# Optimization experiments

Hardware: AMD Instinct MI355X
Metric: run time of the kernel (lower is better)

## Reference

```python
import jax, jax.numpy as jnp
import numpy as np

B, N, C, H = 2, 4096, 384, 6
HD = C // H          # 64
HALF = C // 2        # 192 = 3 pose heads * HD
MLP_H = 4 * C        # 1536
EPS = 1e-5


def _ln(x, g, b):
    m = jnp.mean(x, axis=-1, keepdims=True)
    v = jnp.mean((x - m) ** 2, axis=-1, keepdims=True)
    return (x - m) * jax.lax.rsqrt(v + EPS) * g + b


def setup_inputs() -> dict:
    key = jax.random.key(0)
    ks = jax.random.split(key, 6)
    s = 0.02
    return {
        "x": jax.random.normal(ks[0], (B, N, C), dtype=jnp.float32),
        "qkv_w": jax.random.normal(ks[1], (3 * C, C), dtype=jnp.float32) * s,
        "proj_w": jax.random.normal(ks[2], (C, HALF), dtype=jnp.float32) * s,
        "proj_b": jnp.zeros((C,), jnp.float32),
        "gamma1": jnp.ones((C,), jnp.float32),
        "beta1": jnp.zeros((C,), jnp.float32),
        "gamma2": jnp.ones((C,), jnp.float32),
        "beta2": jnp.zeros((C,), jnp.float32),
        "fc1_w": jax.random.normal(ks[3], (MLP_H, C), dtype=jnp.float32) * s,
        "fc1_b": jnp.zeros((MLP_H,), jnp.float32),
        "fc2_w": jax.random.normal(ks[4], (C, MLP_H), dtype=jnp.float32) * s,
        "fc2_b": jnp.zeros((C,), jnp.float32),
    }


def reference(x, qkv_w, proj_w, proj_b, gamma1, beta1, gamma2, beta2,
              fc1_w, fc1_b, fc2_w, fc2_b):
    b, n, c = x.shape
    scale = HD ** -0.5
    # --- attention on pre-norm input ---
    h = _ln(x, gamma1, beta1)
    qkv = (h @ qkv_w.T).reshape(b, n, 3, H, HD).transpose(2, 0, 3, 1, 4)  # [3,B,H,N,HD]
    q, k, v = qkv[0], qkv[1], qkv[2]
    # obj heads 0:3 -> sigmoid attention; pose heads 3:6 -> softmax attention
    attn_obj = jax.nn.sigmoid(jnp.einsum('bhnd,bhmd->bhnm', q[:, :3], k[:, :3]) * scale)
    attn_pose = jax.nn.softmax(jnp.einsum('bhnd,bhmd->bhnm', q[:, 3:], k[:, 3:]) * scale, axis=-1)
    # chained combine: pose-attn applied after obj-attn on pose values
    ctx = jnp.einsum('bhnm,bhmd->bhnd', attn_obj, v[:, 3:])      # [B,3,N,HD]
    ctx = jnp.einsum('bhnm,bhmd->bhnd', attn_pose, ctx)          # [B,3,N,HD]
    ctx = ctx.transpose(0, 2, 1, 3).reshape(b, n, HALF)          # [B,N,C/2]
    x = x + (ctx @ proj_w.T + proj_b)
    # --- MLP ---
    h2 = _ln(x, gamma2, beta2)
    mlp = jax.nn.gelu(h2 @ fc1_w.T + fc1_b, approximate=False) @ fc2_w.T + fc2_b
    return (x + mlp, attn_obj)
```

## Files before the change

### kernel.cpp

```cpp
#include <hip/hip_runtime.h>
#include <hip/hip_bf16.h>
#include <cmath>


typedef __hip_bfloat16 bf16;
typedef __attribute__((ext_vector_type(8))) short short8;
typedef __attribute__((ext_vector_type(4))) short s16x4;
typedef __attribute__((ext_vector_type(4))) float f32x4;

#define MFMA16(a, b, c) __builtin_amdgcn_mfma_f32_16x16x32_bf16((a), (b), (c), 0, 0, 0)

__device__ __forceinline__ void async16(const void* g, void* l) {
  __builtin_amdgcn_global_load_lds(
      (const __attribute__((address_space(1))) void*)g,
      (__attribute__((address_space(3))) void*)l, 16, 0, 0);
}

__device__ __forceinline__ short f2bs(float v) {
  union { bf16 b; short s; } u;
  u.b = __float2bfloat16(v);
  return u.s;
}

template <bool FIRST>
__global__ __launch_bounds__(256) void ln_fwd(const float* __restrict__ x,
                                              const float* __restrict__ gamma,
                                              const float* __restrict__ beta,
                                              bf16* __restrict__ out,
                                              const float* __restrict__ w0,
                                              const float* __restrict__ w1,
                                              const float* __restrict__ w2,
                                              const float* __restrict__ w3,
                                              bf16* __restrict__ o0, bf16* __restrict__ o1,
                                              bf16* __restrict__ o2, bf16* __restrict__ o3) {
  const int bx = blockIdx.x;
  if (FIRST) {
    if (bx >= 2048) {
      int i = (bx - 2048) * 256 + threadIdx.x;
      const int n0 = 442368 / 4, n1 = 73728 / 4, n2 = 589824 / 4, n3 = 589824 / 4;
      const float* src;
      bf16* dst;
      if (i < n0) { src = w0; dst = o0; }
      else if ((i -= n0) < n1) { src = w1; dst = o1; }
      else if ((i -= n1) < n2) { src = w2; dst = o2; }
      else { i -= n2; src = w3; dst = o3; }
      f32x4 v = *(const f32x4*)(src + (size_t)i * 4);
      s16x4 o;
#pragma unroll
      for (int e = 0; e < 4; ++e) o[e] = f2bs(v[e]);
      *(s16x4*)(dst + (size_t)i * 4) = o;
      return;
    }
  }
  const int row = bx * 4 + (threadIdx.x >> 6);
  const int l = threadIdx.x & 63;
  const float* xr = x + (size_t)row * 384;
  float v[6];
  float s = 0.f, q = 0.f;
#pragma unroll
  for (int i = 0; i < 6; ++i) {
    v[i] = xr[l + i * 64];
    s += v[i];
    q += v[i] * v[i];
  }
#pragma unroll
  for (int m = 1; m < 64; m <<= 1) {
    s += __shfl_xor(s, m);
    q += __shfl_xor(q, m);
  }
  float mean = s * (1.0f / 384.0f);
  float var = q * (1.0f / 384.0f) - mean * mean;
  float rstd = rsqrtf(var + 1e-5f);
  bf16* orow = out + (size_t)row * 384;
#pragma unroll
  for (int i = 0; i < 6; ++i)
    orow[l + i * 64] = __float2bfloat16((v[i] - mean) * rstd * gamma[l + i * 64] + beta[l + i * 64]);
}

template <int EPI>
__global__ __launch_bounds__(256) void gemm128(const bf16* __restrict__ A,
                                               const bf16* __restrict__ Bm, int M, int N, int K,
                                               const float* __restrict__ bias,
                                               bf16* __restrict__ outb) {
  __shared__ __attribute__((aligned(16))) short As[128][64];
  __shared__ __attribute__((aligned(16))) short Bs[128][64];
  const int t = threadIdx.x;
  const int l = t & 63;
  const int w = t >> 6;
  const int wm = w >> 1, wn = w & 1;
  const int bm = blockIdx.y * 128, bn = blockIdx.x * 128;

  f32x4 acc[4][4] = {};
  const int r8 = t >> 3;
  const int c8 = (t & 7) * 8;
  const bf16* Ab = A + (size_t)(bm + r8) * K + c8;
  const bf16* Bb = Bm + (size_t)(bn + r8) * K + c8;

  for (int kt = 0; kt < K; kt += 64) {
    __syncthreads();
#pragma unroll
    for (int i = 0; i < 4; ++i)
      async16(Ab + (size_t)(i * 32) * K + kt, &As[i * 32 + r8][c8]);
#pragma unroll
    for (int i = 0; i < 4; ++i)
      async16(Bb + (size_t)(i * 32) * K + kt, &Bs[i * 32 + r8][c8]);
    __syncthreads();
#pragma unroll
    for (int ks = 0; ks < 2; ++ks) {
      short8 a[4], b[4];
#pragma unroll
      for (int i = 0; i < 4; ++i)
        a[i] = *(const short8*)&As[wm * 64 + i * 16 + (l & 15)][ks * 32 + (l >> 4) * 8];
#pragma unroll
      for (int i = 0; i < 4; ++i)
        b[i] = *(const short8*)&Bs[wn * 64 + i * 16 + (l & 15)][ks * 32 + (l >> 4) * 8];
#pragma unroll
      for (int i = 0; i < 4; ++i)
#pragma unroll
        for (int j = 0; j < 4; ++j) acc[i][j] = MFMA16(a[i], b[j], acc[i][j]);
    }
  }

#pragma unroll
  for (int i = 0; i < 4; ++i) {
#pragma unroll
    for (int j = 0; j < 4; ++j) {
#pragma unroll
      for (int r = 0; r < 4; ++r) {
        int row = bm + wm * 64 + i * 16 + (l >> 4) * 4 + r;
        int col = bn + wn * 64 + j * 16 + (l & 15);
        float v = acc[i][j][r];
        if (EPI == 0) {
          int three = col / 384;
          int rem = col - three * 384;
          int head = rem >> 6;
          int hd = rem & 63;
          int bb = row >> 12;
          int n = row & 4095;
          const size_t QSZ = (size_t)2 * 6 * 4096 * 64;
          if (three < 2) {
            size_t di = ((((size_t)three * 2 + bb) * 6 + head) * 4096 + n) * 64 + hd;
            outb[di] = __float2bfloat16(v);
          } else {
            size_t di = 2 * QSZ + (((size_t)bb * 6 + head) * 64 + hd) * 4096 + n;
            outb[di] = __float2bfloat16(v);
          }
        } else {
          float u = v + bias[col];
          float z = 0.7978845608f * (u + 0.044715f * u * u * u);
          float e = __builtin_amdgcn_exp2f(z * 2.885390082f);
          float th = 1.0f - 2.0f * __builtin_amdgcn_rcpf(e + 1.0f);
          outb[(size_t)row * N + col] = __float2bfloat16(0.5f * u * (1.0f + th));
        }
      }
    }
  }
}

__global__ __launch_bounds__(256) void gemm64sq(const bf16* __restrict__ A,
                                                const bf16* __restrict__ Bm, int M, int N, int K,
                                                const float* __restrict__ bias,
                                                const float* __restrict__ resid,
                                                float* __restrict__ outf) {
  __shared__ __attribute__((aligned(16))) short As[2][64][64];
  __shared__ __attribute__((aligned(16))) short Bs[2][64][64];
  const int t = threadIdx.x;
  const int l = t & 63;
  const int w = t >> 6;
  const int wm = w >> 1, wn = w & 1;
  const int bm = blockIdx.y * 64, bn = blockIdx.x * 64;
  const int r8 = t >> 3, c8 = (t & 7) * 8;

  const bf16* Ab = A + (size_t)(bm + r8) * K + c8;
  const bf16* Bb = Bm + (size_t)(bn + r8) * K + c8;

  f32x4 acc[2][2] = {};

  auto stage = [&](int kt, int bf) {
    async16(Ab + kt, &As[bf][r8][c8]);
    async16(Ab + (size_t)32 * K + kt, &As[bf][32 + r8][c8]);
    async16(Bb + kt, &Bs[bf][r8][c8]);
    async16(Bb + (size_t)32 * K + kt, &Bs[bf][32 + r8][c8]);
  };

  stage(0, 0);
  int bf = 0;
  for (int kt = 0; kt < K; kt += 64) {
    __syncthreads();
    if (kt + 64 < K) stage(kt + 64, bf ^ 1);
#pragma unroll
    for (int ks = 0; ks < 2; ++ks) {
      short8 a[2], b[2];
#pragma unroll
      for (int i = 0; i < 2; ++i)
        a[i] = *(const short8*)&As[bf][wm * 32 + i * 16 + (l & 15)][ks * 32 + (l >> 4) * 8];
#pragma unroll
      for (int j = 0; j < 2; ++j)
        b[j] = *(const short8*)&Bs[bf][wn * 32 + j * 16 + (l & 15)][ks * 32 + (l >> 4) * 8];
#pragma unroll
      for (int i = 0; i < 2; ++i)
#pragma unroll
        for (int j = 0; j < 2; ++j) acc[i][j] = MFMA16(a[i], b[j], acc[i][j]);
    }
    bf ^= 1;
  }

#pragma unroll
  for (int i = 0; i < 2; ++i) {
#pragma unroll
    for (int j = 0; j < 2; ++j) {
#pragma unroll
      for (int r = 0; r < 4; ++r) {
        int row = bm + wm * 32 + i * 16 + (l >> 4) * 4 + r;
        int col = bn + wn * 32 + j * 16 + (l & 15);
        size_t di = (size_t)row * N + col;
        outf[di] = acc[i][j][r] + bias[col] + resid[di];
      }
    }
  }
}

template <int MODE>
__global__ __launch_bounds__(256) void attn_fused(const bf16* __restrict__ qkvb,
                                                  const bf16* __restrict__ vsrc_base,
                                                  float* __restrict__ aout,
                                                  bf16* __restrict__ outd) {
  const int bh = blockIdx.y, b = bh / 3, h = bh - b * 3;
  const int row0 = blockIdx.x * 64;
  const int t = threadIdx.x, l = t & 63, w = t >> 6;

  const size_t HSZ = (size_t)4096 * 64;
  const size_t QSZ = (size_t)2 * 6 * 4096 * 64;
  const int head = (MODE == 0) ? h : h + 3;
  const bf16* qp = qkvb + (size_t)(b * 6 + head) * HSZ;
  const bf16* kp = qkvb + QSZ + (size_t)(b * 6 + head) * HSZ;
  const bf16* vbase = (MODE == 0)
      ? qkvb + 2 * QSZ + (size_t)((b * 6 + h + 3) * 64) * 4096
      : vsrc_base + (size_t)(bh * 64) * 4096;

  __shared__ __attribute__((aligned(16))) short Ks[2][64][64];
  __shared__ __attribute__((aligned(16))) short Vs[2][64][64];
  __shared__ __attribute__((aligned(16))) float Sf[4][16][68];
  __shared__ float Ls[4][16];

  short8 aq[2];
  {
    int qrow = row0 + w * 16 + (l & 15);
    const bf16* qq = qp + (size_t)qrow * 64 + (l >> 4) * 8;
    aq[0] = *(const short8*)(qq);
    aq[1] = *(const short8*)(qq + 32);
  }

  const int r8 = t >> 3, c8 = (t & 7) * 8;
  const int sc = c8 ^ ((r8 & 7) * 8);

  auto stage = [&](int ct, int bf) {
    const bf16* kb = kp + (size_t)(ct * 64) * 64;
    async16(kb + (size_t)r8 * 64 + sc, &Ks[bf][r8][c8]);
    async16(kb + (size_t)(32 + r8) * 64 + sc, &Ks[bf][32 + r8][c8]);
    const bf16* vb = vbase + ct * 64;
    async16(vb + (size_t)r8 * 4096 + sc, &Vs[bf][r8][c8]);
    async16(vb + (size_t)(32 + r8) * 4096 + sc, &Vs[bf][32 + r8][c8]);
  };

  f32x4 cacc[4] = {};
  float lp[4] = {0.f, 0.f, 0.f, 0.f};
  const float K1 = -0.18033688f;
  const float K2 = 0.18033688f;

  float* sfw = &Sf[w][0][0];
  stage(0, 0);
  int bf = 0;
  for (int ct = 0; ct < 64; ++ct) {
    __syncthreads();
    if (ct < 63) stage(ct + 1, bf ^ 1);

    f32x4 sacc[4] = {};
#pragma unroll
    for (int ks = 0; ks < 2; ++ks) {
      short8 bk[4];
#pragma unroll
      for (int j = 0; j < 4; ++j) {
        int rr = j * 16 + (l & 15);
        int ec = (ks * 32 + (l >> 4) * 8) ^ ((rr & 7) * 8);
        bk[j] = *(const short8*)&Ks[bf][rr][ec];
      }
      __builtin_amdgcn_s_setprio(1);
#pragma unroll
      for (int j = 0; j < 4; ++j) sacc[j] = MFMA16(aq[ks], bk[j], sacc[j]);
      __builtin_amdgcn_s_setprio(0);
    }

#pragma unroll
    for (int j = 0; j < 4; ++j) {
#pragma unroll
      for (int r = 0; r < 4; ++r) {
        float s = sacc[j][r];
        float v;
        if (MODE == 0) {
          v = __builtin_amdgcn_rcpf(1.0f + __builtin_amdgcn_exp2f(s * K1));
        } else {
          v = __builtin_amdgcn_exp2f(s * K2);
          lp[r] += v;
        }
        sfw[((l >> 4) * 4 + r) * 68 + j * 16 + (l & 15)] = v;
      }
    }

    short8 pa[2];
#pragma unroll
    for (int ks = 0; ks < 2; ++ks) {
      const float* sp = &sfw[(l & 15) * 68 + ks * 32 + (l >> 4) * 8];
      f32x4 f0 = *(const f32x4*)sp;
      f32x4 f1 = *(const f32x4*)(sp + 4);
      short8 a;
#pragma unroll
      for (int e = 0; e < 4; ++e) a[e] = f2bs(f0[e]);
#pragma unroll
      for (int e = 0; e < 4; ++e) a[4 + e] = f2bs(f1[e]);
      pa[ks] = a;
    }

    if (MODE == 0) {
      float* ab = aout + (size_t)bh * 4096 * 4096 +
                  (size_t)(row0 + w * 16) * 4096 + ct * 64;
#pragma unroll
      for (int i = 0; i < 4; ++i) {
        f32x4 vv = *(const f32x4*)&sfw[(4 * i + (l >> 4)) * 68 + (l & 15) * 4];
        *(f32x4*)(ab + (size_t)(4 * i + (l >> 4)) * 4096 + (l & 15) * 4) = vv;
      }
    }

#pragma unroll
    for (int ks = 0; ks < 2; ++ks) {
      short8 bv[4];
#pragma unroll
      for (int j = 0; j < 4; ++j) {
        int rr = j * 16 + (l & 15);
        int ec = (ks * 32 + (l >> 4) * 8) ^ ((rr & 7) * 8);
        bv[j] = *(const short8*)&Vs[bf][rr][ec];
      }
      __builtin_amdgcn_s_setprio(1);
#pragma unroll
      for (int j = 0; j < 4; ++j) cacc[j] = MFMA16(pa[ks], bv[j], cacc[j]);
      __builtin_amdgcn_s_setprio(0);
    }
    bf ^= 1;
  }

  if (MODE == 0) {
    __syncthreads();
    short(*S)[66] = (short(*)[66]) & Ks[0][0][0];
#pragma unroll
    for (int j = 0; j < 4; ++j)
#pragma unroll
      for (int r = 0; r < 4; ++r)
        S[w * 16 + (l >> 4) * 4 + r][j * 16 + (l & 15)] = f2bs(cacc[j][r]);
    __syncthreads();
    const int hd = t >> 2, nb = (t & 3) * 16;
    short8 o0, o1;
#pragma unroll
    for (int k = 0; k < 8; ++k) o0[k] = S[nb + k][hd];
#pragma unroll
    for (int k = 0; k < 8; ++k) o1[k] = S[nb + 8 + k][hd];
    short* dst = (short*)(outd + ((size_t)bh * 64 + hd) * 4096 + row0 + nb);
    *(short8*)dst = o0;
    *(short8*)(dst + 8) = o1;
  } else {
#pragma unroll
    for (int r = 0; r < 4; ++r) {
#pragma unroll
      for (int m = 1; m < 16; m <<= 1) lp[r] += __shfl_xor(lp[r], m);
    }
    if ((l & 15) == 0) {
#pragma unroll
      for (int r = 0; r < 4; ++r) Ls[w][(l >> 4) * 4 + r] = lp[r];
    }
#pragma unroll
    for (int j = 0; j < 4; ++j)
#pragma unroll
      for (int r = 0; r < 4; ++r)
        sfw[((l >> 4) * 4 + r) * 68 + j * 16 + (l & 15)] = cacc[j][r];
    const int row = l >> 2, hd0 = (l & 3) * 16;
    float inv = 1.0f / Ls[w][row];
    short8 o[2];
#pragma unroll
    for (int g = 0; g < 4; ++g) {
      f32x4 v = *(const f32x4*)&sfw[row * 68 + hd0 + g * 4];
#pragma unroll
      for (int e = 0; e < 4; ++e) o[g >> 1][(g & 1) * 4 + e] = f2bs(v[e] * inv);
    }
    short* dst = (short*)(outd + ((size_t)b * 4096 + row0 + w * 16 + row) * 192 + h * 64 + hd0);
    *(short8*)dst = o[0];
    *(short8*)(dst + 8) = o[1];
  }
}

extern "C" void kernel_launch(void* const* d_in, const int* in_sizes, int n_in,
                              void* d_out, int out_size, void* d_ws, size_t ws_size,
                              hipStream_t stream) {
  const float* x      = (const float*)d_in[0];
  const float* qkv_w  = (const float*)d_in[1];
  const float* proj_w = (const float*)d_in[2];
  const float* proj_b = (const float*)d_in[3];
  const float* gamma1 = (const float*)d_in[4];
  const float* beta1  = (const float*)d_in[5];
  const float* gamma2 = (const float*)d_in[6];
  const float* beta2  = (const float*)d_in[7];
  const float* fc1_w  = (const float*)d_in[8];
  const float* fc1_b  = (const float*)d_in[9];
  const float* fc2_w  = (const float*)d_in[10];
  const float* fc2_b  = (const float*)d_in[11];

  float* out_x = (float*)d_out;
  float* out_attn = out_x + (size_t)2 * 4096 * 384;

  char* ws = (char*)d_ws;
  size_t off = 0;
  auto alloc = [&](size_t bytes) -> void* {
    void* p = ws + off;
    off += (bytes + 255) & ~(size_t)255;
    return p;
  };
  bf16* qkv_w_b  = (bf16*)alloc((size_t)1152 * 384 * 2);
  bf16* proj_w_b = (bf16*)alloc((size_t)384 * 192 * 2);
  bf16* fc1_w_b  = (bf16*)alloc((size_t)1536 * 384 * 2);
  bf16* fc2_w_b  = (bf16*)alloc((size_t)384 * 1536 * 2);
  bf16* h1    = (bf16*)alloc((size_t)8192 * 384 * 2);
  bf16* qkvb  = (bf16*)alloc((size_t)3 * 2 * 6 * 4096 * 64 * 2);
  bf16* ctx1T = (bf16*)alloc((size_t)6 * 64 * 4096 * 2);
  bf16* ctxf  = (bf16*)alloc((size_t)2 * 4096 * 192 * 2);
  float* x2   = (float*)alloc((size_t)8192 * 384 * 4);
  bf16* h2    = (bf16*)alloc((size_t)8192 * 384 * 2);
  bf16* h3    = (bf16*)alloc((size_t)8192 * 1536 * 2);

  ln_fwd<true><<<3704, 256, 0, stream>>>(x, gamma1, beta1, h1,
                                         qkv_w, proj_w, fc1_w, fc2_w,
                                         qkv_w_b, proj_w_b, fc1_w_b, fc2_w_b);

  gemm128<0><<<dim3(9, 64), 256, 0, stream>>>(h1, qkv_w_b, 8192, 1152, 384,
                                              nullptr, qkvb);

  attn_fused<0><<<dim3(64, 6), 256, 0, stream>>>(qkvb, nullptr, out_attn, ctx1T);
  attn_fused<1><<<dim3(64, 6), 256, 0, stream>>>(qkvb, ctx1T, nullptr, ctxf);

  gemm64sq<<<dim3(6, 128), 256, 0, stream>>>(ctxf, proj_w_b, 8192, 384, 192,
                                             proj_b, x, x2);
  ln_fwd<false><<<2048, 256, 0, stream>>>(x2, gamma2, beta2, h2,
                                          nullptr, nullptr, nullptr, nullptr,
                                          nullptr, nullptr, nullptr, nullptr);
  gemm128<2><<<dim3(12, 64), 256, 0, stream>>>(h2, fc1_w_b, 8192, 1536, 384,
                                               fc1_b, h3);
  gemm64sq<<<dim3(6, 128), 256, 0, stream>>>(h3, fc2_w_b, 8192, 384, 1536,
                                             fc2_b, x2, out_x);
}
```

Measured before the change: 309.0 us.

## Split pose softmax attention over key chunks with partial-sum reduction kernel

The softmax pose attention kernel is split out and parallelised across four key chunks, so the grid grows from 384 to 1536 blocks, which should fill the GPU better. Each block writes unnormalised partial context and row sums, and a new reduce kernel combines them and normalises. The pose kernel also drops LDS staging of K and V and reads fragments straight from global memory. This adds extra fp32 partial-buffer traffic and a kernel launch. Skipping the max subtraction was already the approach before, so numerics are unchanged.

Measured after the change: 417.0 us. 1.35x slower.

```diff
diff --git a/kernel.cpp b/kernel.cpp
--- a/kernel.cpp
+++ b/kernel.cpp
@@ -220,28 +220,22 @@
   }
 }
 
-template <int MODE>
-__global__ __launch_bounds__(256) void attn_fused(const bf16* __restrict__ qkvb,
-                                                  const bf16* __restrict__ vsrc_base,
-                                                  float* __restrict__ aout,
-                                                  bf16* __restrict__ outd) {
+__global__ __launch_bounds__(256) void attn_obj(const bf16* __restrict__ qkvb,
+                                                float* __restrict__ aout,
+                                                bf16* __restrict__ ctx1T) {
   const int bh = blockIdx.y, b = bh / 3, h = bh - b * 3;
   const int row0 = blockIdx.x * 64;
   const int t = threadIdx.x, l = t & 63, w = t >> 6;
 
   const size_t HSZ = (size_t)4096 * 64;
   const size_t QSZ = (size_t)2 * 6 * 4096 * 64;
-  const int head = (MODE == 0) ? h : h + 3;
-  const bf16* qp = qkvb + (size_t)(b * 6 + head) * HSZ;
-  const bf16* kp = qkvb + QSZ + (size_t)(b * 6 + head) * HSZ;
-  const bf16* vbase = (MODE == 0)
-      ? qkvb + 2 * QSZ + (size_t)((b * 6 + h + 3) * 64) * 4096
-      : vsrc_base + (size_t)(bh * 64) * 4096;
+  const bf16* qp = qkvb + (size_t)(b * 6 + h) * HSZ;
+  const bf16* kp = qkvb + QSZ + (size_t)(b * 6 + h) * HSZ;
+  const bf16* vbase = qkvb + 2 * QSZ + (size_t)((b * 6 + h + 3) * 64) * 4096;
 
   __shared__ __attribute__((aligned(16))) short Ks[2][64][64];
   __shared__ __attribute__((aligned(16))) short Vs[2][64][64];
   __shared__ __attribute__((aligned(16))) float Sf[4][16][68];
-  __shared__ float Ls[4][16];
 
   short8 aq[2];
   {
@@ -264,9 +258,7 @@
   };
 
   f32x4 cacc[4] = {};
-  float lp[4] = {0.f, 0.f, 0.f, 0.f};
   const float K1 = -0.18033688f;
-  const float K2 = 0.18033688f;
 
   float* sfw = &Sf[w][0][0];
   stage(0, 0);
@@ -295,14 +287,7 @@
     for (int j = 0; j < 4; ++j) {
 #pragma unroll
       for (int r = 0; r < 4; ++r) {
-        float s = sacc[j][r];
-        float v;
-        if (MODE == 0) {
-          v = __builtin_amdgcn_rcpf(1.0f + __builtin_amdgcn_exp2f(s * K1));
-        } else {
-          v = __builtin_amdgcn_exp2f(s * K2);
-          lp[r] += v;
-        }
+        float v = __builtin_amdgcn_rcpf(1.0f + __builtin_amdgcn_exp2f(sacc[j][r] * K1));
         sfw[((l >> 4) * 4 + r) * 68 + j * 16 + (l & 15)] = v;
       }
     }
@@ -321,7 +306,7 @@
       pa[ks] = a;
     }
 
-    if (MODE == 0) {
+    {
       float* ab = aout + (size_t)bh * 4096 * 4096 +
                   (size_t)(row0 + w * 16) * 4096 + ct * 64;
 #pragma unroll
@@ -348,52 +333,154 @@
     bf ^= 1;
   }
 
-  if (MODE == 0) {
-    __syncthreads();
-    short(*S)[66] = (short(*)[66]) & Ks[0][0][0];
-#pragma unroll
-    for (int j = 0; j < 4; ++j)
-#pragma unroll
-      for (int r = 0; r < 4; ++r)
-        S[w * 16 + (l >> 4) * 4 + r][j * 16 + (l & 15)] = f2bs(cacc[j][r]);
-    __syncthreads();
-    const int hd = t >> 2, nb = (t & 3) * 16;
-    short8 o0, o1;
-#pragma unroll
-    for (int k = 0; k < 8; ++k) o0[k] = S[nb + k][hd];
-#pragma unroll
-    for (int k = 0; k < 8; ++k) o1[k] = S[nb + 8 + k][hd];
-    short* dst = (short*)(outd + ((size_t)bh * 64 + hd) * 4096 + row0 + nb);
-    *(short8*)dst = o0;
-    *(short8*)(dst + 8) = o1;
-  } else {
-#pragma unroll
-    for (int r = 0; r < 4; ++r) {
-#pragma unroll
-      for (int m = 1; m < 16; m <<= 1) lp[r] += __shfl_xor(lp[r], m);
-    }
-    if ((l & 15) == 0) {
-#pragma unroll
-      for (int r = 0; r < 4; ++r) Ls[w][(l >> 4) * 4 + r] = lp[r];
-    }
-#pragma unroll
-    for (int j = 0; j < 4; ++j)
-#pragma unroll
-      for (int r = 0; r < 4; ++r)
-        sfw[((l >> 4) * 4 + r) * 68 + j * 16 + (l & 15)] = cacc[j][r];
-    const int row = l >> 2, hd0 = (l & 3) * 16;
-    float inv = 1.0f / Ls[w][row];
-    short8 o[2];
-#pragma unroll
-    for (int g = 0; g < 4; ++g) {
-      f32x4 v = *(const f32x4*)&sfw[row * 68 + hd0 + g * 4];
-#pragma unroll
-      for (int e = 0; e < 4; ++e) o[g >> 1][(g & 1) * 4 + e] = f2bs(v[e] * inv);
-    }
-    short* dst = (short*)(outd + ((size_t)b * 4096 + row0 + w * 16 + row) * 192 + h * 64 + hd0);
-    *(short8*)dst = o[0];
-    *(short8*)(dst + 8) = o[1];
-  }
+  __syncthreads();
+  short(*S)[66] = (short(*)[66]) & Ks[0][0][0];
+#pragma unroll
+  for (int j = 0; j < 4; ++j)
+#pragma unroll
+    for (int r = 0; r < 4; ++r)
+      S[w * 16 + (l >> 4) * 4 + r][j * 16 + (l & 15)] = f2bs(cacc[j][r]);
+  __syncthreads();
+  const int hd = t >> 2, nb = (t & 3) * 16;
+  short8 o0, o1;
+#pragma unroll
+  for (int k = 0; k < 8; ++k) o0[k] = S[nb + k][hd];
+#pragma unroll
+  for (int k = 0; k < 8; ++k) o1[k] = S[nb + 8 + k][hd];
+  short* dst = (short*)(ctx1T + ((size_t)bh * 64 + hd) * 4096 + row0 + nb);
+  *(short8*)dst = o0;
+  *(short8*)(dst + 8) = o1;
+}
+
+__global__ __launch_bounds__(256) void attn_pose(const bf16* __restrict__ qkvb,
+                                                 const bf16* __restrict__ ctx1T,
+                                                 float* __restrict__ part,
+                                                 float* __restrict__ lpart) {
+  const int bh = blockIdx.z, b = bh / 3, h = bh - b * 3;
+  const int row0 = blockIdx.x * 64;
+  const int cbase = blockIdx.y * 1024;
+  const int t = threadIdx.x, l = t & 63, w = t >> 6;
+
+  const size_t HSZ = (size_t)4096 * 64;
+  const size_t QSZ = (size_t)2 * 6 * 4096 * 64;
+  const bf16* qp = qkvb + (size_t)(b * 6 + h + 3) * HSZ;
+  const bf16* kp = qkvb + QSZ + (size_t)(b * 6 + h + 3) * HSZ;
+  const bf16* vbase = ctx1T + (size_t)(bh * 64) * 4096;
+
+  __shared__ __attribute__((aligned(16))) float Sf[4][16][68];
+
+  short8 aq[2];
+  {
+    int qrow = row0 + w * 16 + (l & 15);
+    const bf16* qq = qp + (size_t)qrow * 64 + (l >> 4) * 8;
+    aq[0] = *(const short8*)(qq);
+    aq[1] = *(const short8*)(qq + 32);
+  }
+
+  f32x4 cacc[4] = {};
+  float lp[4] = {0.f, 0.f, 0.f, 0.f};
+  const float K2 = 0.18033688f;
+
+  const bf16* kfp = kp + (size_t)(cbase + (l & 15)) * 64 + (l >> 4) * 8;
+  const bf16* vfp = vbase + (size_t)(l & 15) * 4096 + cbase + (l >> 4) * 8;
+
+  float* sfw = &Sf[w][0][0];
+  for (int ct = 0; ct < 16; ++ct) {
+    f32x4 sacc[4] = {};
+    short8 bk[2][4];
+#pragma unroll
+    for (int ks = 0; ks < 2; ++ks)
+#pragma unroll
+      for (int j = 0; j < 4; ++j)
+        bk[ks][j] = *(const short8*)(kfp + (size_t)(ct * 64 + j * 16) * 64 + ks * 32);
+#pragma unroll
+    for (int ks = 0; ks < 2; ++ks) {
+      __builtin_amdgcn_s_setprio(1);
+#pragma unroll
+      for (int j = 0; j < 4; ++j) sacc[j] = MFMA16(aq[ks], bk[ks][j], sacc[j]);
+      __builtin_amdgcn_s_setprio(0);
+    }
+
+    short8 bv[2][4];
+#pragma unroll
+    for (int ks = 0; ks < 2; ++ks)
+#pragma unroll
+      for (int j = 0; j < 4; ++j)
+        bv[ks][j] = *(const short8*)(vfp + (size_t)(j * 16) * 4096 + ct * 64 + ks * 32);
+
+#pragma unroll
+    for (int j = 0; j < 4; ++j) {
+#pragma unroll
+      for (int r = 0; r < 4; ++r) {
+        float v = __builtin_amdgcn_exp2f(sacc[j][r] * K2);
+        lp[r] += v;
+        sfw[((l >> 4) * 4 + r) * 68 + j * 16 + (l & 15)] = v;
+      }
+    }
+
+    short8 pa[2];
+#pragma unroll
+    for (int ks = 0; ks < 2; ++ks) {
+      const float* sp = &sfw[(l & 15) * 68 + ks * 32 + (l >> 4) * 8];
+      f32x4 f0 = *(const f32x4*)sp;
+      f32x4 f1 = *(const f32x4*)(sp + 4);
+      short8 a;
+#pragma unroll
+      for (int e = 0; e < 4; ++e) a[e] = f2bs(f0[e]);
+#pragma unroll
+      for (int e = 0; e < 4; ++e) a[4 + e] = f2bs(f1[e]);
+      pa[ks] = a;
+    }
+
+#pragma unroll
+    for (int ks = 0; ks < 2; ++ks) {
+      __builtin_amdgcn_s_setprio(1);
+#pragma unroll
+      for (int j = 0; j < 4; ++j) cacc[j] = MFMA16(pa[ks], bv[ks][j], cacc[j]);
+      __builtin_amdgcn_s_setprio(0);
+    }
+  }
+
+  float* pb = part + ((size_t)(blockIdx.y * 6 + bh) * 4096 + row0 + w * 16) * 64;
+#pragma unroll
+  for (int j = 0; j < 4; ++j)
+#pragma unroll
+    for (int r = 0; r < 4; ++r)
+      pb[(size_t)((l >> 4) * 4 + r) * 64 + j * 16 + (l & 15)] = cacc[j][r];
+
+#pragma unroll
+  for (int r = 0; r < 4; ++r) {
+#pragma unroll
+    for (int m = 1; m < 16; m <<= 1) lp[r] += __shfl_xor(lp[r], m);
+  }
+  if ((l & 15) == 0) {
+    float* lb = lpart + (size_t)(blockIdx.y * 6 + bh) * 4096 + row0 + w * 16 + (l >> 4) * 4;
+#pragma unroll
+    for (int r = 0; r < 4; ++r) lb[r] = lp[r];
+  }
+}
+
+__global__ __launch_bounds__(256) void reduce_pose(const float* __restrict__ part,
+                                                   const float* __restrict__ lpart,
+                                                   bf16* __restrict__ ctxf) {
+  const int idx = blockIdx.x * 256 + threadIdx.x;
+  const int hd4 = idx & 15;
+  const int n = (idx >> 4) & 4095;
+  const int bh = idx >> 16;
+  const size_t CS = (size_t)6 * 4096 * 64, CL = (size_t)6 * 4096;
+  f32x4 s = {};
+  float lt = 0.f;
+#pragma unroll
+  for (int c = 0; c < 4; ++c) {
+    s += *(const f32x4*)(part + c * CS + ((size_t)bh * 4096 + n) * 64 + hd4 * 4);
+    lt += lpart[c * CL + (size_t)bh * 4096 + n];
+  }
+  float inv = 1.0f / lt;
+  int b = bh / 3, h = bh - b * 3;
+  s16x4 o;
+#pragma unroll
+  for (int e = 0; e < 4; ++e) o[e] = f2bs(s[e] * inv);
+  *(s16x4*)(ctxf + ((size_t)b * 4096 + n) * 192 + h * 64 + hd4 * 4) = o;
 }
 
 extern "C" void kernel_launch(void* const* d_in, const int* in_sizes, int n_in,
@@ -428,6 +515,8 @@
   bf16* fc2_w_b  = (bf16*)alloc((size_t)384 * 1536 * 2);
   bf16* h1    = (bf16*)alloc((size_t)8192 * 384 * 2);
   bf16* qkvb  = (bf16*)alloc((size_t)3 * 2 * 6 * 4096 * 64 * 2);
+  float* cpp  = (float*)alloc((size_t)4 * 6 * 4096 * 64 * 4);
+  float* lpp  = (float*)alloc((size_t)4 * 6 * 4096 * 4);
   bf16* ctx1T = (bf16*)alloc((size_t)6 * 64 * 4096 * 2);
   bf16* ctxf  = (bf16*)alloc((size_t)2 * 4096 * 192 * 2);
   float* x2   = (float*)alloc((size_t)8192 * 384 * 4);
@@ -441,8 +530,9 @@
   gemm128<0><<<dim3(9, 64), 256, 0, stream>>>(h1, qkv_w_b, 8192, 1152, 384,
                                               nullptr, qkvb);
 
-  attn_fused<0><<<dim3(64, 6), 256, 0, stream>>>(qkvb, nullptr, out_attn, ctx1T);
-  attn_fused<1><<<dim3(64, 6), 256, 0, stream>>>(qkvb, ctx1T, nullptr, ctxf);
+  attn_obj<<<dim3(64, 6), 256, 0, stream>>>(qkvb, out_attn, ctx1T);
+  attn_pose<<<dim3(64, 4, 6), 256, 0, stream>>>(qkvb, ctx1T, cpp, lpp);
+  reduce_pose<<<1536, 256, 0, stream>>>(cpp, lpp, ctxf);
 
   gemm64sq<<<dim3(6, 128), 256, 0, stream>>>(ctxf, proj_w_b, 8192, 384, 192,
                                              proj_b, x, x2);
```
